# Performance work log

Measured on AMD Instinct MI355X. Metric: run time of the kernel, lower is better.

Reference implementation:

```python
import jax, jax.numpy as jnp
import numpy as np
from jax import lax

B, S, H, T = 64, 512, 1024, 21


def setup_inputs() -> dict:
    key = jax.random.key(0)
    k1, k2, k3, k4, k5, k6, k7 = jax.random.split(key, 7)
    hidden_states = jax.random.normal(k1, (B, S, H), dtype=jnp.float32)
    attention_mask = jnp.ones((B, S), dtype=jnp.int32)
    labels = jax.random.randint(k2, (B, S), 0, T).astype(jnp.int64)
    W = jax.random.normal(k3, (T, H), dtype=jnp.float32) * 0.02
    b = jnp.zeros((T,), dtype=jnp.float32)
    # torchcrf init: uniform(-0.1, 0.1)
    transitions = jax.random.uniform(k4, (T, T), minval=-0.1, maxval=0.1, dtype=jnp.float32)
    start_transitions = jax.random.uniform(k5, (T,), minval=-0.1, maxval=0.1, dtype=jnp.float32)
    end_transitions = jax.random.uniform(k6, (T,), minval=-0.1, maxval=0.1, dtype=jnp.float32)
    return {
        "hidden_states": hidden_states,
        "attention_mask": attention_mask,
        "labels": labels,
        "W": W,
        "b": b,
        "transitions": transitions,
        "start_transitions": start_transitions,
        "end_transitions": end_transitions,
    }


def _crf_log_likelihood(emissions, labels, mask, trans, start, end):
    # emissions [B,S,T], labels [B,S] int, mask [B,S] bool. reduction='sum'.
    Bn, Sn, Tn = emissions.shape
    maskf = mask.astype(emissions.dtype)
    emit_scores = jnp.take_along_axis(emissions, labels[:, :, None], axis=2)[:, :, 0]  # [B,S]
    trans_scores = trans[labels[:, :-1], labels[:, 1:]]  # [B,S-1]
    numerator = start[labels[:, 0]] + emit_scores[:, 0]
    numerator = numerator + jnp.sum((trans_scores + emit_scores[:, 1:]) * maskf[:, 1:], axis=1)
    seq_ends = jnp.sum(mask.astype(jnp.int32), axis=1) - 1  # [B]
    last_tags = labels[jnp.arange(Bn), seq_ends]
    numerator = numerator + end[last_tags]
    # partition via forward algorithm (scan over time)
    alpha0 = start[None, :] + emissions[:, 0]  # [B,T]
    def step(alpha, inp):
        emit_t, mask_t = inp  # [B,T], [B]
        nxt = jax.nn.logsumexp(alpha[:, :, None] + trans[None, :, :] + emit_t[:, None, :], axis=1)
        return jnp.where(mask_t[:, None], nxt, alpha), None
    alpha, _ = lax.scan(step, alpha0, (emissions[:, 1:].transpose(1, 0, 2), mask[:, 1:].T))
    log_Z = jax.nn.logsumexp(alpha + end[None, :], axis=1)  # [B]
    return jnp.sum(numerator - log_Z)


def _viterbi_decode(emissions, mask, trans, start, end):
    Bn, Sn, Tn = emissions.shape
    score0 = start[None, :] + emissions[:, 0]  # [B,T]
    identity_bp = jnp.broadcast_to(jnp.arange(Tn)[None, :], (Bn, Tn))
    def fwd(score, inp):
        emit_t, mask_t = inp
        broad = score[:, :, None] + trans[None, :, :]  # [B, prev, cur]
        best_prev = jnp.argmax(broad, axis=1)  # [B,T]
        nxt = jnp.max(broad, axis=1) + emit_t
        new_score = jnp.where(mask_t[:, None], nxt, score)
        bp = jnp.where(mask_t[:, None], best_prev, identity_bp)
        return new_score, bp
    final_score, bps = lax.scan(fwd, score0, (emissions[:, 1:].transpose(1, 0, 2), mask[:, 1:].T))
    last_tag = jnp.argmax(final_score + end[None, :], axis=1)  # [B] tag at pos S-1
    def back(tag, bp_t):
        prev = jnp.take_along_axis(bp_t, tag[:, None], axis=1)[:, 0]
        return prev, tag
    tag0, tags_rest = lax.scan(back, last_tag, bps, reverse=True)  # tags_rest[t] = tag at pos t+1
    tags = jnp.concatenate([tag0[None, :], tags_rest], axis=0).T  # [B,S]
    return jnp.where(mask, tags, 0).astype(jnp.int64)


def reference(hidden_states, attention_mask, labels, W, b, transitions, start_transitions, end_transitions):
    mask = attention_mask.astype(bool)
    # dropout is identity in eval mode
    emissions = jnp.einsum("bsh,th->bst", hidden_states, W) + b  # [B,S,T]
    log_prob = _crf_log_likelihood(emissions, labels, mask, transitions, start_transitions, end_transitions)
    loss = -log_prob
    pred = _viterbi_decode(emissions, mask, transitions, start_transitions, end_transitions)
    return loss, pred
```

## Files before the change

kernel.cpp:

```cpp
#include <hip/hip_runtime.h>
#include <math.h>
#include <stdint.h>

#define BB 64
#define SS 512
#define HH 1024
#define TT 21

template <int CTRL>
__device__ __forceinline__ float dpp_add(float v) {
  int t = __builtin_amdgcn_update_dpp(0, __float_as_int(v), CTRL, 0xF, 0xF, true);
  return v + __int_as_float(t);
}
__device__ __forceinline__ float wave_sum(float v) {
  v = dpp_add<0x121>(v);
  v = dpp_add<0x122>(v);
  v = dpp_add<0x124>(v);
  v = dpp_add<0x128>(v);
  v += __shfl_xor(v, 16);
  v += __shfl_xor(v, 32);
  return v;
}

#define DOT4(A, H, WV)    \
  A = fmaf(H.x, WV.x, A); \
  A = fmaf(H.y, WV.y, A); \
  A = fmaf(H.z, WV.z, A); \
  A = fmaf(H.w, WV.w, A)

__global__ __launch_bounds__(192) void k_emis(const float* __restrict__ hs,
                                              const float* __restrict__ W,
                                              const float* __restrict__ bias,
                                              float* __restrict__ emis) {
  __shared__ float part[192 * 7];
  const int tid = threadIdx.x;
  const int q = tid & 7;
  const int tmp = tid >> 3;
  const int tg = tmp % 3;
  const int r = tmp / 3;
  const size_t row = (size_t)blockIdx.x * 8 + r;
  const float4* hp = (const float4*)(hs + row * HH);
  const float* wb0 = W + (size_t)(tg * 7) * HH + q * 4;

  float acc[7] = {0.f, 0.f, 0.f, 0.f, 0.f, 0.f, 0.f};
  float4 h = hp[q];
  for (int i = 0; i < 32; ++i) {
    const float4 hc = h;
    if (i < 31) h = hp[(i + 1) * 8 + q];
    const float* wb = wb0 + (size_t)i * 32;
#pragma unroll
    for (int lt = 0; lt < 7; ++lt) {
      const float4 w = *(const float4*)(wb + (size_t)lt * HH);
      DOT4(acc[lt], hc, w);
    }
  }
#pragma unroll
  for (int lt = 0; lt < 7; ++lt) part[tid * 7 + lt] = acc[lt];
  __syncthreads();

  if (tid < 8 * TT) {
    const int rr = tid / TT;
    const int t = tid - rr * TT;
    const int tg2 = t / 7;
    const int lt2 = t - tg2 * 7;
    const float* pp = part + ((rr * 3 + tg2) * 8) * 7 + lt2;
    float s = ((pp[0] + pp[7]) + (pp[14] + pp[21])) +
              ((pp[28] + pp[35]) + (pp[42] + pp[49]));
    emis[(size_t)blockIdx.x * (8 * TT) + tid] = s + bias[t];
  }
}

#define RLF(V, K) __int_as_float(__builtin_amdgcn_readlane(__float_as_int(V), K))

__global__ __launch_bounds__(64, 1) void k_scan(const float* __restrict__ emis,
                                                const int* __restrict__ mask,
                                                const float* __restrict__ trans,
                                                const float* __restrict__ sv,
                                                const float* __restrict__ ev,
                                                float* __restrict__ logZ,
                                                float* __restrict__ pred) {
  __shared__ float sE[SS * TT];
  __shared__ int sM[SS];
  __shared__ unsigned char bp[SS][32];
  __shared__ unsigned char sTag[SS];
  const int lane = threadIdx.x;
  const int j = lane;
  const bool act = (j < TT);
  const int jj = act ? j : 0;
  const int b = blockIdx.x & 63;

  {
    const float4* src = (const float4*)(emis + (size_t)b * SS * TT);
    float4* dst = (float4*)sE;
    for (int i = lane; i < SS * TT / 4; i += 64) dst[i] = src[i];
    const int* msrc = mask + b * SS;
    for (int i = lane; i < SS; i += 64) sM[i] = msrc[i];
  }
  __syncthreads();

  if (blockIdx.x < 64) {
    float E[TT];
#pragma unroll
    for (int i = 0; i < TT; ++i) E[i] = __expf(trans[i * TT + jj]);
    float v = act ? __expf(sv[jj] + sE[jj]) : 0.f;
    float C = 0.f;
    float ge_nx = __expf(sE[TT + jj]);
    int mk_nx = sM[1];
    for (int t = 1; t < SS; ++t) {
      const float ge = ge_nx;
      const int mk = mk_nx;
      const int tn = (t + 1 < SS) ? (t + 1) : (SS - 1);
      ge_nx = __expf(sE[tn * TT + jj]);
      mk_nx = sM[tn];
      const float v0 = RLF(v, 0), v1 = RLF(v, 1), v2 = RLF(v, 2);
      const float v3 = RLF(v, 3), v4 = RLF(v, 4), v5 = RLF(v, 5);
      const float v6 = RLF(v, 6), v7 = RLF(v, 7), v8 = RLF(v, 8);
      const float v9 = RLF(v, 9), v10 = RLF(v, 10), v11 = RLF(v, 11);
      const float v12 = RLF(v, 12), v13 = RLF(v, 13), v14 = RLF(v, 14);
      const float v15 = RLF(v, 15), v16 = RLF(v, 16), v17 = RLF(v, 17);
      const float v18 = RLF(v, 18), v19 = RLF(v, 19), v20 = RLF(v, 20);
      float scale = 1.0f;
      if ((t & 7) == 0) {
        float m = fmaxf(fmaxf(fmaxf(v0, v1), fmaxf(v2, v3)),
                        fmaxf(fmaxf(v4, v5), fmaxf(v6, v7)));
        m = fmaxf(m, fmaxf(fmaxf(v8, v9), fmaxf(v10, v11)));
        m = fmaxf(m, fmaxf(fmaxf(v12, v13), fmaxf(v14, v15)));
        m = fmaxf(m, fmaxf(fmaxf(v16, v17), fmaxf(v18, v19)));
        m = fmaxf(m, v20);
        int ex = (int)((__float_as_uint(m) >> 23) & 255u) - 127;
        scale = __uint_as_float((unsigned)(127 - ex) << 23);
        C += (float)ex * 0.6931471805599453f;
        v *= scale;
      }
      float q0 = v0 * E[0], q1 = v1 * E[1], q2 = v2 * E[2];
      q0 = fmaf(v3, E[3], q0);   q1 = fmaf(v4, E[4], q1);   q2 = fmaf(v5, E[5], q2);
      q0 = fmaf(v6, E[6], q0);   q1 = fmaf(v7, E[7], q1);   q2 = fmaf(v8, E[8], q2);
      q0 = fmaf(v9, E[9], q0);   q1 = fmaf(v10, E[10], q1); q2 = fmaf(v11, E[11], q2);
      q0 = fmaf(v12, E[12], q0); q1 = fmaf(v13, E[13], q1); q2 = fmaf(v14, E[14], q2);
      q0 = fmaf(v15, E[15], q0); q1 = fmaf(v16, E[16], q1); q2 = fmaf(v17, E[17], q2);
      q0 = fmaf(v18, E[18], q0); q1 = fmaf(v19, E[19], q1); q2 = fmaf(v20, E[20], q2);
      float vn = ((q0 + q1 + q2) * scale) * ge;
      v = (act && mk) ? vn : v;
    }
    float wv = act ? v * __expf(ev[jj]) : 0.f;
#pragma unroll
    for (int d = 32; d >= 1; d >>= 1) wv += __shfl_xor(wv, d);
    if (lane == 0) logZ[b] = C + __logf(wv);
  } else {
    float Tc[TT];
#pragma unroll
    for (int i = 0; i < TT; ++i) Tc[i] = trans[i * TT + jj];
    float sc = act ? (sv[jj] + sE[jj]) : -3.0e38f;
    float e_nx = sE[TT + jj];
    int mk_nx = sM[1];
    for (int t = 1; t < SS; ++t) {
      const float e = e_nx;
      const int mk = mk_nx;
      const int tn = (t + 1 < SS) ? (t + 1) : (SS - 1);
      e_nx = sE[tn * TT + jj];
      mk_nx = sM[tn];
      const float s0 = RLF(sc, 0), s1 = RLF(sc, 1), s2 = RLF(sc, 2);
      const float s3 = RLF(sc, 3), s4 = RLF(sc, 4), s5 = RLF(sc, 5);
      const float s6 = RLF(sc, 6), s7 = RLF(sc, 7), s8 = RLF(sc, 8);
      const float s9 = RLF(sc, 9), s10 = RLF(sc, 10), s11 = RLF(sc, 11);
      const float s12 = RLF(sc, 12), s13 = RLF(sc, 13), s14 = RLF(sc, 14);
      const float s15 = RLF(sc, 15), s16 = RLF(sc, 16), s17 = RLF(sc, 17);
      const float s18 = RLF(sc, 18), s19 = RLF(sc, 19), s20 = RLF(sc, 20);
      float b0v, b1v, b2v;
      int i0, i1, i2;
#define ARGSTEP(BV, BI, VAL, IDX)          \
  {                                        \
    float x_ = (VAL) + Tc[IDX];            \
    if (x_ > BV) { BV = x_; BI = (IDX); }  \
  }
      b0v = s0 + Tc[0]; i0 = 0;
      b1v = s1 + Tc[1]; i1 = 1;
      b2v = s2 + Tc[2]; i2 = 2;
      ARGSTEP(b0v, i0, s3, 3);   ARGSTEP(b1v, i1, s4, 4);   ARGSTEP(b2v, i2, s5, 5);
      ARGSTEP(b0v, i0, s6, 6);   ARGSTEP(b1v, i1, s7, 7);   ARGSTEP(b2v, i2, s8, 8);
      ARGSTEP(b0v, i0, s9, 9);   ARGSTEP(b1v, i1, s10, 10); ARGSTEP(b2v, i2, s11, 11);
      ARGSTEP(b0v, i0, s12, 12); ARGSTEP(b1v, i1, s13, 13); ARGSTEP(b2v, i2, s14, 14);
      ARGSTEP(b0v, i0, s15, 15); ARGSTEP(b1v, i1, s16, 16); ARGSTEP(b2v, i2, s17, 17);
      ARGSTEP(b0v, i0, s18, 18); ARGSTEP(b1v, i1, s19, 19); ARGSTEP(b2v, i2, s20, 20);
#undef ARGSTEP
      float best = b0v;
      int bi = i0;
      if (b1v > best || (b1v == best && i1 < bi)) { best = b1v; bi = i1; }
      if (b2v > best || (b2v == best && i2 < bi)) { best = b2v; bi = i2; }
      float ns = best + e;
      sc = (act && mk) ? ns : sc;
      if (act) bp[t][j] = (unsigned char)(mk ? bi : j);
    }
    float fsv = act ? (sc + ev[jj]) : -3.0e38f;
    int idx = j;
#pragma unroll
    for (int d = 32; d >= 1; d >>= 1) {
      float ov = __shfl_xor(fsv, d);
      int oi = __shfl_xor(idx, d);
      bool take = (ov > fsv) || (ov == fsv && oi < idx);
      fsv = take ? ov : fsv;
      idx = take ? oi : idx;
    }
    __syncthreads();
    if (lane == 0) {
      int tag = idx;
      sTag[SS - 1] = (unsigned char)tag;
      for (int t = SS - 1; t >= 1; --t) {
        tag = bp[t][tag];
        sTag[t - 1] = (unsigned char)tag;
      }
    }
    __syncthreads();
    for (int i = lane; i < SS; i += 64) {
      pred[(size_t)b * SS + i] = (float)(sM[i] ? (int)sTag[i] : 0);
    }
  }
}

__global__ __launch_bounds__(64, 1) void k_loss(const float* __restrict__ emis,
                                                const int* __restrict__ mask,
                                                const int* __restrict__ labels,
                                                const float* __restrict__ trans,
                                                const float* __restrict__ sv,
                                                const float* __restrict__ ev,
                                                const float* __restrict__ logZ,
                                                float* __restrict__ outv) {
  const int b = blockIdx.x;
  const int lane = threadIdx.x;
  float p = 0.f;
  int cnt = 0;
  for (int t = lane; t < SS; t += 64) {
    cnt += mask[b * SS + t] ? 1 : 0;
    if (t >= 1) {
      const int lp = labels[b * SS + t - 1];
      const int lc = labels[b * SS + t];
      const float mk = (float)mask[b * SS + t];
      p += mk * (trans[lp * TT + lc] + emis[((size_t)b * SS + t) * TT + lc]);
    }
  }
  p = wave_sum(p);
#pragma unroll
  for (int d = 32; d >= 1; d >>= 1) cnt += __shfl_xor(cnt, d);
  if (lane == 0) {
    const int l0 = labels[b * SS];
    float numer = p + sv[l0] + emis[(size_t)b * SS * TT + l0];
    numer += ev[labels[b * SS + cnt - 1]];
    atomicAdd(outv, logZ[b] - numer);
  }
}

extern "C" void kernel_launch(void* const* d_in, const int* in_sizes, int n_in,
                              void* d_out, int out_size, void* d_ws, size_t ws_size,
                              hipStream_t stream) {
  const float* hs = (const float*)d_in[0];
  const int* msk = (const int*)d_in[1];
  const int* lab = (const int*)d_in[2];
  const float* W = (const float*)d_in[3];
  const float* bias = (const float*)d_in[4];
  const float* trans = (const float*)d_in[5];
  const float* sv = (const float*)d_in[6];
  const float* ev = (const float*)d_in[7];
  float* out = (float*)d_out;

  float* emis = (float*)d_ws;
  float* logZ = emis + (size_t)BB * SS * TT;

  hipMemsetAsync(d_out, 0, 4, stream);
  k_emis<<<4096, 192, 0, stream>>>(hs, W, bias, emis);
  k_scan<<<128, 64, 0, stream>>>(emis, msk, trans, sv, ev, logZ, out + 1);
  k_loss<<<64, 64, 0, stream>>>(emis, msk, lab, trans, sv, ev, logZ, out);
}
```

Measured before the change: 526.3 us.

## Process two rows per thread in emission GEMV and stream emissions in scan

The emission kernel now computes two hidden-state rows per thread so each W load is reused twice, and launches half as many blocks with a launch-bounds occupancy hint. The scan kernel drops the upfront copy of the whole per-batch emission slab and mask into LDS. Instead it prefetches emissions from global memory in chunks of 8 timesteps and reads masks as int4 vectors. This is meant to remove the serial LDS staging latency at scan start and halve W traffic, at the cost of more registers and global-latency exposure inside the recurrence.

```diff
diff --git a/kernel.cpp b/kernel.cpp
--- a/kernel.cpp
+++ b/kernel.cpp
@@ -28,45 +28,55 @@
   A = fmaf(H.z, WV.z, A); \
   A = fmaf(H.w, WV.w, A)
 
-__global__ __launch_bounds__(192) void k_emis(const float* __restrict__ hs,
-                                              const float* __restrict__ W,
-                                              const float* __restrict__ bias,
-                                              float* __restrict__ emis) {
-  __shared__ float part[192 * 7];
+__global__ __launch_bounds__(192, 4) void k_emis(const float* __restrict__ hs,
+                                                 const float* __restrict__ W,
+                                                 const float* __restrict__ bias,
+                                                 float* __restrict__ emis) {
+  __shared__ float part[192 * 14];
   const int tid = threadIdx.x;
   const int q = tid & 7;
   const int tmp = tid >> 3;
   const int tg = tmp % 3;
-  const int r = tmp / 3;
-  const size_t row = (size_t)blockIdx.x * 8 + r;
-  const float4* hp = (const float4*)(hs + row * HH);
+  const int rp = tmp / 3;
+  const size_t row0 = (size_t)blockIdx.x * 16 + rp * 2;
+  const float4* hp0 = (const float4*)(hs + row0 * HH);
+  const float4* hp1 = (const float4*)(hs + (row0 + 1) * HH);
   const float* wb0 = W + (size_t)(tg * 7) * HH + q * 4;
 
-  float acc[7] = {0.f, 0.f, 0.f, 0.f, 0.f, 0.f, 0.f};
-  float4 h = hp[q];
+  float a0[7] = {0.f, 0.f, 0.f, 0.f, 0.f, 0.f, 0.f};
+  float a1[7] = {0.f, 0.f, 0.f, 0.f, 0.f, 0.f, 0.f};
+  float4 h0 = hp0[q], h1 = hp1[q];
+#pragma unroll 2
   for (int i = 0; i < 32; ++i) {
-    const float4 hc = h;
-    if (i < 31) h = hp[(i + 1) * 8 + q];
+    const float4 hc0 = h0, hc1 = h1;
+    if (i < 31) {
+      h0 = hp0[(i + 1) * 8 + q];
+      h1 = hp1[(i + 1) * 8 + q];
+    }
     const float* wb = wb0 + (size_t)i * 32;
 #pragma unroll
     for (int lt = 0; lt < 7; ++lt) {
       const float4 w = *(const float4*)(wb + (size_t)lt * HH);
-      DOT4(acc[lt], hc, w);
-    }
-  }
-#pragma unroll
-  for (int lt = 0; lt < 7; ++lt) part[tid * 7 + lt] = acc[lt];
+      DOT4(a0[lt], hc0, w);
+      DOT4(a1[lt], hc1, w);
+    }
+  }
+#pragma unroll
+  for (int lt = 0; lt < 7; ++lt) {
+    part[tid * 14 + lt] = a0[lt];
+    part[tid * 14 + 7 + lt] = a1[lt];
+  }
   __syncthreads();
 
-  if (tid < 8 * TT) {
-    const int rr = tid / TT;
-    const int t = tid - rr * TT;
+  for (int o = tid; o < 16 * TT; o += 192) {
+    const int rr = o / TT;
+    const int t = o - rr * TT;
     const int tg2 = t / 7;
     const int lt2 = t - tg2 * 7;
-    const float* pp = part + ((rr * 3 + tg2) * 8) * 7 + lt2;
-    float s = ((pp[0] + pp[7]) + (pp[14] + pp[21])) +
-              ((pp[28] + pp[35]) + (pp[42] + pp[49]));
-    emis[(size_t)blockIdx.x * (8 * TT) + tid] = s + bias[t];
+    const float* pp = part + (((rr >> 1) * 3 + tg2) * 8) * 14 + (rr & 1) * 7 + lt2;
+    float s = ((pp[0] + pp[14]) + (pp[28] + pp[42])) +
+              ((pp[56] + pp[70]) + (pp[84] + pp[98]));
+    emis[(size_t)blockIdx.x * (16 * TT) + o] = s + bias[t];
   }
 }
 
@@ -79,8 +89,6 @@
                                                 const float* __restrict__ ev,
                                                 float* __restrict__ logZ,
                                                 float* __restrict__ pred) {
-  __shared__ float sE[SS * TT];
-  __shared__ int sM[SS];
   __shared__ unsigned char bp[SS][32];
   __shared__ unsigned char sTag[SS];
   const int lane = threadIdx.x;
@@ -88,59 +96,74 @@
   const bool act = (j < TT);
   const int jj = act ? j : 0;
   const int b = blockIdx.x & 63;
-
-  {
-    const float4* src = (const float4*)(emis + (size_t)b * SS * TT);
-    float4* dst = (float4*)sE;
-    for (int i = lane; i < SS * TT / 4; i += 64) dst[i] = src[i];
-    const int* msrc = mask + b * SS;
-    for (int i = lane; i < SS; i += 64) sM[i] = msrc[i];
-  }
-  __syncthreads();
+  const float* eb = emis + (size_t)b * SS * TT + jj;
+  const int4* mq = (const int4*)(mask + b * SS);
 
   if (blockIdx.x < 64) {
     float E[TT];
 #pragma unroll
     for (int i = 0; i < TT; ++i) E[i] = __expf(trans[i * TT + jj]);
-    float v = act ? __expf(sv[jj] + sE[jj]) : 0.f;
+    float v = act ? __expf(sv[jj] + eb[0]) : 0.f;
     float C = 0.f;
-    float ge_nx = __expf(sE[TT + jj]);
-    int mk_nx = sM[1];
-    for (int t = 1; t < SS; ++t) {
-      const float ge = ge_nx;
-      const int mk = mk_nx;
-      const int tn = (t + 1 < SS) ? (t + 1) : (SS - 1);
-      ge_nx = __expf(sE[tn * TT + jj]);
-      mk_nx = sM[tn];
-      const float v0 = RLF(v, 0), v1 = RLF(v, 1), v2 = RLF(v, 2);
-      const float v3 = RLF(v, 3), v4 = RLF(v, 4), v5 = RLF(v, 5);
-      const float v6 = RLF(v, 6), v7 = RLF(v, 7), v8 = RLF(v, 8);
-      const float v9 = RLF(v, 9), v10 = RLF(v, 10), v11 = RLF(v, 11);
-      const float v12 = RLF(v, 12), v13 = RLF(v, 13), v14 = RLF(v, 14);
-      const float v15 = RLF(v, 15), v16 = RLF(v, 16), v17 = RLF(v, 17);
-      const float v18 = RLF(v, 18), v19 = RLF(v, 19), v20 = RLF(v, 20);
-      float scale = 1.0f;
-      if ((t & 7) == 0) {
-        float m = fmaxf(fmaxf(fmaxf(v0, v1), fmaxf(v2, v3)),
-                        fmaxf(fmaxf(v4, v5), fmaxf(v6, v7)));
-        m = fmaxf(m, fmaxf(fmaxf(v8, v9), fmaxf(v10, v11)));
-        m = fmaxf(m, fmaxf(fmaxf(v12, v13), fmaxf(v14, v15)));
-        m = fmaxf(m, fmaxf(fmaxf(v16, v17), fmaxf(v18, v19)));
-        m = fmaxf(m, v20);
-        int ex = (int)((__float_as_uint(m) >> 23) & 255u) - 127;
-        scale = __uint_as_float((unsigned)(127 - ex) << 23);
-        C += (float)ex * 0.6931471805599453f;
-        v *= scale;
-      }
-      float q0 = v0 * E[0], q1 = v1 * E[1], q2 = v2 * E[2];
-      q0 = fmaf(v3, E[3], q0);   q1 = fmaf(v4, E[4], q1);   q2 = fmaf(v5, E[5], q2);
-      q0 = fmaf(v6, E[6], q0);   q1 = fmaf(v7, E[7], q1);   q2 = fmaf(v8, E[8], q2);
-      q0 = fmaf(v9, E[9], q0);   q1 = fmaf(v10, E[10], q1); q2 = fmaf(v11, E[11], q2);
-      q0 = fmaf(v12, E[12], q0); q1 = fmaf(v13, E[13], q1); q2 = fmaf(v14, E[14], q2);
-      q0 = fmaf(v15, E[15], q0); q1 = fmaf(v16, E[16], q1); q2 = fmaf(v17, E[17], q2);
-      q0 = fmaf(v18, E[18], q0); q1 = fmaf(v19, E[19], q1); q2 = fmaf(v20, E[20], q2);
-      float vn = ((q0 + q1 + q2) * scale) * ge;
-      v = (act && mk) ? vn : v;
+    float pre[8], cur[8];
+#pragma unroll
+    for (int k = 0; k < 8; ++k) pre[k] = eb[(size_t)(1 + k) * TT];
+    int4 qA = mq[0];
+    for (int c = 0; c < 64; ++c) {
+      const int base = c * 8;
+      const int4 qB = mq[2 * c + 1];
+      const int4 qC = mq[(2 * c + 2 < 128) ? (2 * c + 2) : 127];
+      float ge[8];
+#pragma unroll
+      for (int k = 0; k < 8; ++k) cur[k] = pre[k];
+#pragma unroll
+      for (int k = 0; k < 8; ++k) ge[k] = __expf(cur[k]);
+      if (c < 63) {
+#pragma unroll
+        for (int k = 0; k < 8; ++k) {
+          int tl = base + 9 + k;
+          tl = (tl < SS) ? tl : (SS - 1);
+          pre[k] = eb[(size_t)tl * TT];
+        }
+      }
+      const int mks[8] = {qA.y, qA.z, qA.w, qB.x, qB.y, qB.z, qB.w, qC.x};
+#pragma unroll
+      for (int p = 0; p < 8; ++p) {
+        const int t = base + 1 + p;
+        if (t >= SS) break;
+        const int mk = mks[p];
+        const float ge_t = ge[p];
+        const float v0 = RLF(v, 0), v1 = RLF(v, 1), v2 = RLF(v, 2);
+        const float v3 = RLF(v, 3), v4 = RLF(v, 4), v5 = RLF(v, 5);
+        const float v6 = RLF(v, 6), v7 = RLF(v, 7), v8 = RLF(v, 8);
+        const float v9 = RLF(v, 9), v10 = RLF(v, 10), v11 = RLF(v, 11);
+        const float v12 = RLF(v, 12), v13 = RLF(v, 13), v14 = RLF(v, 14);
+        const float v15 = RLF(v, 15), v16 = RLF(v, 16), v17 = RLF(v, 17);
+        const float v18 = RLF(v, 18), v19 = RLF(v, 19), v20 = RLF(v, 20);
+        float scale = 1.0f;
+        if (p == 7) {
+          float m = fmaxf(fmaxf(fmaxf(v0, v1), fmaxf(v2, v3)),
+                          fmaxf(fmaxf(v4, v5), fmaxf(v6, v7)));
+          m = fmaxf(m, fmaxf(fmaxf(v8, v9), fmaxf(v10, v11)));
+          m = fmaxf(m, fmaxf(fmaxf(v12, v13), fmaxf(v14, v15)));
+          m = fmaxf(m, fmaxf(fmaxf(v16, v17), fmaxf(v18, v19)));
+          m = fmaxf(m, v20);
+          int ex = (int)((__float_as_uint(m) >> 23) & 255u) - 127;
+          scale = __uint_as_float((unsigned)(127 - ex) << 23);
+          C += (float)ex * 0.6931471805599453f;
+          v *= scale;
+        }
+        float q0 = v0 * E[0], q1 = v1 * E[1], q2 = v2 * E[2];
+        q0 = fmaf(v3, E[3], q0);   q1 = fmaf(v4, E[4], q1);   q2 = fmaf(v5, E[5], q2);
+        q0 = fmaf(v6, E[6], q0);   q1 = fmaf(v7, E[7], q1);   q2 = fmaf(v8, E[8], q2);
+        q0 = fmaf(v9, E[9], q0);   q1 = fmaf(v10, E[10], q1); q2 = fmaf(v11, E[11], q2);
+        q0 = fmaf(v12, E[12], q0); q1 = fmaf(v13, E[13], q1); q2 = fmaf(v14, E[14], q2);
+        q0 = fmaf(v15, E[15], q0); q1 = fmaf(v16, E[16], q1); q2 = fmaf(v17, E[17], q2);
+        q0 = fmaf(v18, E[18], q0); q1 = fmaf(v19, E[19], q1); q2 = fmaf(v20, E[20], q2);
+        float vn = ((q0 + q1 + q2) * scale) * ge_t;
+        v = (act && mk) ? vn : v;
+      }
+      qA = qC;
     }
     float wv = act ? v * __expf(ev[jj]) : 0.f;
 #pragma unroll
@@ -150,46 +173,65 @@
     float Tc[TT];
 #pragma unroll
     for (int i = 0; i < TT; ++i) Tc[i] = trans[i * TT + jj];
-    float sc = act ? (sv[jj] + sE[jj]) : -3.0e38f;
-    float e_nx = sE[TT + jj];
-    int mk_nx = sM[1];
-    for (int t = 1; t < SS; ++t) {
-      const float e = e_nx;
-      const int mk = mk_nx;
-      const int tn = (t + 1 < SS) ? (t + 1) : (SS - 1);
-      e_nx = sE[tn * TT + jj];
-      mk_nx = sM[tn];
-      const float s0 = RLF(sc, 0), s1 = RLF(sc, 1), s2 = RLF(sc, 2);
-      const float s3 = RLF(sc, 3), s4 = RLF(sc, 4), s5 = RLF(sc, 5);
-      const float s6 = RLF(sc, 6), s7 = RLF(sc, 7), s8 = RLF(sc, 8);
-      const float s9 = RLF(sc, 9), s10 = RLF(sc, 10), s11 = RLF(sc, 11);
-      const float s12 = RLF(sc, 12), s13 = RLF(sc, 13), s14 = RLF(sc, 14);
-      const float s15 = RLF(sc, 15), s16 = RLF(sc, 16), s17 = RLF(sc, 17);
-      const float s18 = RLF(sc, 18), s19 = RLF(sc, 19), s20 = RLF(sc, 20);
-      float b0v, b1v, b2v;
-      int i0, i1, i2;
+    float sc = act ? (sv[jj] + eb[0]) : -3.0e38f;
+    float pre[8], cur[8];
+#pragma unroll
+    for (int k = 0; k < 8; ++k) pre[k] = eb[(size_t)(1 + k) * TT];
+    int4 qA = mq[0];
+    for (int c = 0; c < 64; ++c) {
+      const int base = c * 8;
+      const int4 qB = mq[2 * c + 1];
+      const int4 qC = mq[(2 * c + 2 < 128) ? (2 * c + 2) : 127];
+#pragma unroll
+      for (int k = 0; k < 8; ++k) cur[k] = pre[k];
+      if (c < 63) {
+#pragma unroll
+        for (int k = 0; k < 8; ++k) {
+          int tl = base + 9 + k;
+          tl = (tl < SS) ? tl : (SS - 1);
+          pre[k] = eb[(size_t)tl * TT];
+        }
+      }
+      const int mks[8] = {qA.y, qA.z, qA.w, qB.x, qB.y, qB.z, qB.w, qC.x};
+#pragma unroll
+      for (int p = 0; p < 8; ++p) {
+        const int t = base + 1 + p;
+        if (t >= SS) break;
+        const int mk = mks[p];
+        const float e = cur[p];
+        const float s0 = RLF(sc, 0), s1 = RLF(sc, 1), s2 = RLF(sc, 2);
+        const float s3 = RLF(sc, 3), s4 = RLF(sc, 4), s5 = RLF(sc, 5);
+        const float s6 = RLF(sc, 6), s7 = RLF(sc, 7), s8 = RLF(sc, 8);
+        const float s9 = RLF(sc, 9), s10 = RLF(sc, 10), s11 = RLF(sc, 11);
+        const float s12 = RLF(sc, 12), s13 = RLF(sc, 13), s14 = RLF(sc, 14);
+        const float s15 = RLF(sc, 15), s16 = RLF(sc, 16), s17 = RLF(sc, 17);
+        const float s18 = RLF(sc, 18), s19 = RLF(sc, 19), s20 = RLF(sc, 20);
+        float b0v, b1v, b2v;
+        int i0, i1, i2;
 #define ARGSTEP(BV, BI, VAL, IDX)          \
   {                                        \
     float x_ = (VAL) + Tc[IDX];            \
     if (x_ > BV) { BV = x_; BI = (IDX); }  \
   }
-      b0v = s0 + Tc[0]; i0 = 0;
-      b1v = s1 + Tc[1]; i1 = 1;
-      b2v = s2 + Tc[2]; i2 = 2;
-      ARGSTEP(b0v, i0, s3, 3);   ARGSTEP(b1v, i1, s4, 4);   ARGSTEP(b2v, i2, s5, 5);
-      ARGSTEP(b0v, i0, s6, 6);   ARGSTEP(b1v, i1, s7, 7);   ARGSTEP(b2v, i2, s8, 8);
-      ARGSTEP(b0v, i0, s9, 9);   ARGSTEP(b1v, i1, s10, 10); ARGSTEP(b2v, i2, s11, 11);
-      ARGSTEP(b0v, i0, s12, 12); ARGSTEP(b1v, i1, s13, 13); ARGSTEP(b2v, i2, s14, 14);
-      ARGSTEP(b0v, i0, s15, 15); ARGSTEP(b1v, i1, s16, 16); ARGSTEP(b2v, i2, s17, 17);
-      ARGSTEP(b0v, i0, s18, 18); ARGSTEP(b1v, i1, s19, 19); ARGSTEP(b2v, i2, s20, 20);
+        b0v = s0 + Tc[0]; i0 = 0;
+        b1v = s1 + Tc[1]; i1 = 1;
+        b2v = s2 + Tc[2]; i2 = 2;
+        ARGSTEP(b0v, i0, s3, 3);   ARGSTEP(b1v, i1, s4, 4);   ARGSTEP(b2v, i2, s5, 5);
+        ARGSTEP(b0v, i0, s6, 6);   ARGSTEP(b1v, i1, s7, 7);   ARGSTEP(b2v, i2, s8, 8);
+        ARGSTEP(b0v, i0, s9, 9);   ARGSTEP(b1v, i1, s10, 10); ARGSTEP(b2v, i2, s11, 11);
+        ARGSTEP(b0v, i0, s12, 12); ARGSTEP(b1v, i1, s13, 13); ARGSTEP(b2v, i2, s14, 14);
+        ARGSTEP(b0v, i0, s15, 15); ARGSTEP(b1v, i1, s16, 16); ARGSTEP(b2v, i2, s17, 17);
+        ARGSTEP(b0v, i0, s18, 18); ARGSTEP(b1v, i1, s19, 19); ARGSTEP(b2v, i2, s20, 20);
 #undef ARGSTEP
-      float best = b0v;
-      int bi = i0;
-      if (b1v > best || (b1v == best && i1 < bi)) { best = b1v; bi = i1; }
-      if (b2v > best || (b2v == best && i2 < bi)) { best = b2v; bi = i2; }
-      float ns = best + e;
-      sc = (act && mk) ? ns : sc;
-      if (act) bp[t][j] = (unsigned char)(mk ? bi : j);
+        float best = b0v;
+        int bi = i0;
+        if (b1v > best || (b1v == best && i1 < bi)) { best = b1v; bi = i1; }
+        if (b2v > best || (b2v == best && i2 < bi)) { best = b2v; bi = i2; }
+        float ns = best + e;
+        sc = (act && mk) ? ns : sc;
+        if (act) bp[t][j] = (unsigned char)(mk ? bi : j);
+      }
+      qA = qC;
     }
     float fsv = act ? (sc + ev[jj]) : -3.0e38f;
     int idx = j;
@@ -212,7 +254,7 @@
     }
     __syncthreads();
     for (int i = lane; i < SS; i += 64) {
-      pred[(size_t)b * SS + i] = (float)(sM[i] ? (int)sTag[i] : 0);
+      pred[(size_t)b * SS + i] = (float)(mask[b * SS + i] ? (int)sTag[i] : 0);
     }
   }
 }
@@ -266,7 +308,7 @@
   float* logZ = emis + (size_t)BB * SS * TT;
 
   hipMemsetAsync(d_out, 0, 4, stream);
-  k_emis<<<4096, 192, 0, stream>>>(hs, W, bias, emis);
+  k_emis<<<2048, 192, 0, stream>>>(hs, W, bias, emis);
   k_scan<<<128, 64, 0, stream>>>(emis, msk, trans, sv, ev, logZ, out + 1);
   k_loss<<<64, 64, 0, stream>>>(emis, msk, lab, trans, sv, ev, logZ, out);
 }
```

New measurement: 432.1 us. 17.9% less time.
